# Performance work log

Measured on AMD Instinct MI355X. Metric: run time of the kernel, lower is better.

## Reference

```python
import jax, jax.numpy as jnp
import numpy as np

B, N, F, T, K, O = 8, 1024, 64, 32, 3, 64


def setup_inputs() -> dict:
    key = jax.random.key(0)
    k0, k1, k2, k3 = jax.random.split(key, 4)
    x = jax.random.normal(k0, (B, N, F, T), dtype=jnp.float32)
    spatial_attention = jax.random.uniform(k1, (B, N, N), dtype=jnp.float32)
    cheb = jax.random.normal(k2, (K, N, N), dtype=jnp.float32) * 0.1  # stacked T_k
    Theta = jax.random.normal(k3, (K, F, O), dtype=jnp.float32) * (1.0 / np.sqrt(F))
    return {"x": x, "spatial_attention": spatial_attention, "cheb": cheb, "Theta": Theta}


def reference(x, spatial_attention, cheb, Theta):
    # Original per-timestep, per-k loop computes:
    #   rhs[b,i,f] = sum_j (T_k[j,i] * att[b,j,i])... note: T_k_with_at.permute(0,2,1) @ x
    #   i.e. rhs[b,i,f,t] = sum_j T_k[j,i]*att[b,j,i]*x[b,j,f,t]
    # Vectorized over all timesteps t and Chebyshev orders k at once.
    rhs = jnp.einsum('kji,bji,bjft->bkift', cheb, spatial_attention, x)  # (B,K,N,F,T)
    out = jnp.einsum('bkift,kfo->biot', rhs, Theta)                      # sum over k,f
    return jax.nn.relu(out)  # (B,N,O,T)
```

## Files before the change

### kernel.cpp

```cpp
#include <hip/hip_runtime.h>
#include <stdint.h>

#define Bn 8
#define Nn 1024
#define Fn 64
#define Tn 32
#define Kn 3
#define On 64
#define Rn (Kn * Nn)
#define Cn (On * Tn)
#define NT (Rn / 64)

typedef __bf16 bf16x8 __attribute__((ext_vector_type(8)));
typedef float f32x4 __attribute__((ext_vector_type(4)));
typedef __attribute__((address_space(1))) void gvoid;
typedef __attribute__((address_space(3))) void lvoid;

union BF8 { bf16x8 v; ushort s[8]; uint4 q; };

static __device__ __forceinline__ ushort f2bf(float f) {
  uint32_t u = __float_as_uint(f);
  return (ushort)((u + 0x7FFFu + ((u >> 16) & 1u)) >> 16);
}

static __device__ __forceinline__ void glds(const ushort* g, ushort* l) {
  __builtin_amdgcn_global_load_lds((gvoid*)g, (lvoid*)l, 16, 0, 0);
}

__global__ void k_thetaT(const float* __restrict__ Theta, ushort* __restrict__ ThT) {
  int idx = blockIdx.x * 256 + threadIdx.x;
  if (idx < Kn * On * Fn) {
    int k = idx / (On * Fn);
    int rem = idx % (On * Fn);
    int o = rem / Fn, f = rem % Fn;
    ThT[idx] = f2bf(Theta[(k * Fn + f) * On + o]);
  }
}

__global__ __launch_bounds__(256) void k_prepW(const float* __restrict__ att,
                                               const float* __restrict__ cheb,
                                               ushort* __restrict__ Wt) {
  __shared__ float chebT[Kn][64][33];
  __shared__ float attT[64][33];
  int i0 = blockIdx.x * 64, j0 = blockIdx.y * 32;
  int tid = threadIdx.x;
  int il = tid & 63, jr = tid >> 6;
  int jc = tid & 3, iw = tid >> 2;

#pragma unroll
  for (int k = 0; k < Kn; k++)
#pragma unroll
    for (int p = 0; p < 8; p++) {
      int j = jr + p * 4;
      chebT[k][il][j] = cheb[((size_t)k * Nn + j0 + j) * Nn + i0 + il];
    }

  for (int b = 0; b < Bn; b++) {
    __syncthreads();
#pragma unroll
    for (int p = 0; p < 8; p++) {
      int j = jr + p * 4;
      attT[il][j] = att[((size_t)b * Nn + j0 + j) * Nn + i0 + il];
    }
    __syncthreads();
#pragma unroll
    for (int k = 0; k < Kn; k++) {
      ushort tmp[8];
#pragma unroll
      for (int q = 0; q < 8; q++)
        tmp[q] = f2bf(attT[iw][jc * 8 + q] * chebT[k][iw][jc * 8 + q]);
      *(uint4*)&Wt[((size_t)b * Nn + i0 + iw) * Rn + (size_t)k * Nn + j0 + jc * 8] =
          *(const uint4*)tmp;
    }
  }
}

__global__ __launch_bounds__(512) void k_prepY(const float* __restrict__ x,
                                               const ushort* __restrict__ ThT,
                                               ushort* __restrict__ Yt) {
  __shared__ ushort ylds[1024 * 32];
  int jt = blockIdx.x, b = blockIdx.y;
  int j0 = jt * 32;
  int tid = threadIdx.x;
  int lane = tid & 63, w = tid >> 6;
  int l15 = lane & 15, l4 = lane >> 4;

  BF8 bfr[4][2][2];
#pragma unroll
  for (int jj = 0; jj < 4; jj++) {
    const float* xp = x + ((size_t)b * Nn + (j0 + w * 4 + jj)) * (Fn * Tn);
#pragma unroll
    for (int ks = 0; ks < 2; ks++)
#pragma unroll
      for (int tf = 0; tf < 2; tf++) {
        int t = tf * 16 + l15;
        int fb = ks * 32 + l4 * 8;
#pragma unroll
        for (int e = 0; e < 8; e++)
          bfr[jj][ks][tf].s[e] = f2bf(xp[(fb + e) * Tn + t]);
      }
  }

  for (int k = 0; k < Kn; k++) {
    for (int h = 0; h < 2; h++) {
      BF8 afr[2][2];
#pragma unroll
      for (int o2 = 0; o2 < 2; o2++)
#pragma unroll
        for (int ks = 0; ks < 2; ks++) {
          int o = h * 32 + o2 * 16 + l15;
          afr[o2][ks].q = *(const uint4*)&ThT[((size_t)k * On + o) * Fn + ks * 32 + l4 * 8];
        }
#pragma unroll
      for (int jj = 0; jj < 4; jj++) {
        f32x4 acc[2][2] = {};
#pragma unroll
        for (int ks = 0; ks < 2; ks++)
#pragma unroll
          for (int o2 = 0; o2 < 2; o2++)
#pragma unroll
            for (int tf = 0; tf < 2; tf++)
              acc[o2][tf] = __builtin_amdgcn_mfma_f32_16x16x32_bf16(
                  afr[o2][ks].v, bfr[jj][ks][tf].v, acc[o2][tf], 0, 0, 0);
#pragma unroll
        for (int o2 = 0; o2 < 2; o2++)
#pragma unroll
          for (int tf = 0; tf < 2; tf++)
#pragma unroll
            for (int q = 0; q < 4; q++) {
              int cl = (o2 * 16 + l4 * 4 + q) * Tn + tf * 16 + l15;
              ylds[cl * 32 + w * 4 + jj] = f2bf(acc[o2][tf][q]);
            }
      }
      __syncthreads();
      const uint4* yl4 = (const uint4*)ylds;
      uint4* Yt4 = (uint4*)Yt;
      int e4 = tid & 3, r4 = tid >> 2;
      for (int pass = 0; pass < 8; pass++) {
        int cl = pass * 128 + r4;
        size_t off = ((size_t)b * Cn + (size_t)(h * 1024 + cl)) * Rn + (size_t)k * Nn + j0;
        Yt4[off / 8 + e4] = yl4[cl * 4 + e4];
      }
      __syncthreads();
    }
  }
}

__global__ __launch_bounds__(512, 2) void k_gemm(const ushort* __restrict__ Wt,
                                                 const ushort* __restrict__ Yt,
                                                 float* __restrict__ out) {
  extern __shared__ __align__(16) ushort smem[];
  ushort* As = smem;
  ushort* Bs = smem + 32768;

  int g = blockIdx.x;
  int b = g & 7, slot = g >> 3;
  int i0 = (slot & 3) * 256, c0 = (slot >> 2) * 256;
  int tid = threadIdx.x, lane = tid & 63, w = tid >> 6;
  int l15 = lane & 15, l4 = lane >> 4;
  int wm = w >> 2, wn = w & 3;

  const ushort* Ab = Wt + ((size_t)b * Nn + i0) * Rn;
  const ushort* Bb = Yt + ((size_t)b * Cn + c0) * Rn;

  int srcC = (((lane & 7) ^ (lane >> 3)) * 8);
  int arow0 = w * 8 + (lane >> 3);
  int brow0 = (w >> 2) * 64 + (w & 3) * 8 + (lane >> 3);

  int aL = (wm * 64 + l15) * 64;
  int bL = (wn * 32 + l15) * 64;
  int x7 = l15 & 7;
  int colx0 = ((l4) ^ x7) * 8;
  int colx1 = ((4 + l4) ^ x7) * 8;

  f32x4 acc[8][4] = {};
  BF8 afX[4][2], afY[4][2];
  BF8 bfX[2][2], bfY[2][2];

#define MFMA_(a_, b_, c_) __builtin_amdgcn_mfma_f32_16x16x32_bf16((a_), (b_), (c_), 0, 0, 0)
#define BAR() asm volatile("s_barrier" ::: "memory")
#define PRIO1 __builtin_amdgcn_s_setprio(1)
#define PRIO0 __builtin_amdgcn_s_setprio(0)
#define VMC(n_) asm volatile("s_waitcnt vmcnt(" #n_ ")" ::: "memory")

#define STAGE_A(t_, h_) { int bo_ = ((t_) & 1) * 16384 + (h_) * 8192 + w * 512; \
    const ushort* gp_ = Ab + (size_t)(arow0 + (h_) * 64) * Rn + (t_) * 64 + srcC; \
    glds(gp_, As + bo_); \
    glds(gp_ + 128 * (size_t)Rn, As + bo_ + 4096); }
#define STAGE_B(t_, h_) { int bo_ = ((t_) & 1) * 16384 + (h_) * 8192 + w * 512; \
    const ushort* gp_ = Bb + (size_t)(brow0 + (h_) * 32) * Rn + (t_) * 64 + srcC; \
    glds(gp_, Bs + bo_); \
    glds(gp_ + 128 * (size_t)Rn, Bs + bo_ + 4096); }

#define RD_A(DST_, bo_, mh_) { _Pragma("unroll") for (int m = 0; m < 4; m++) { \
    int ba_ = (bo_) + (mh_) * 8192 + aL + m * 1024; \
    DST_[m][0].q = *(const uint4*)&As[ba_ + colx0]; \
    DST_[m][1].q = *(const uint4*)&As[ba_ + colx1]; } }
#define RD_B(DST_, bo_, nh_) { _Pragma("unroll") for (int n = 0; n < 2; n++) { \
    int bb_ = (bo_) + (nh_) * 8192 + bL + n * 1024; \
    DST_[n][0].q = *(const uint4*)&Bs[bb_ + colx0]; \
    DST_[n][1].q = *(const uint4*)&Bs[bb_ + colx1]; } }

#define MMC(AF_, BF_, MO_, NO_) { _Pragma("unroll") for (int ks = 0; ks < 2; ks++) \
    _Pragma("unroll") for (int m = 0; m < 4; m++) \
      _Pragma("unroll") for (int n = 0; n < 2; n++) \
        acc[(MO_) + m][(NO_) + n] = MFMA_(AF_[m][ks].v, BF_[n][ks].v, acc[(MO_) + m][(NO_) + n]); }

  STAGE_A(0, 0); STAGE_B(0, 0); STAGE_B(0, 1); STAGE_A(0, 1); STAGE_A(1, 0);
  VMC(6); BAR();
  RD_A(afX, 0, 0); RD_B(bfX, 0, 0);

#define TILE(t_, S0_, S1_, S2_, W0_, W1_, W3_, LAST_) { \
    int bo_c = ((t_) & 1) * 16384; \
    VMC(W0_); BAR(); \
    RD_B(bfY, bo_c, 1); \
    if (S0_) STAGE_B((t_) + 1, 0); \
    PRIO1; MMC(afX, bfX, 0, 0); PRIO0; \
    VMC(W1_); BAR(); \
    RD_A(afY, bo_c, 1); \
    if (S1_) { STAGE_B((t_) + 1, 1); STAGE_A((t_) + 1, 1); } \
    PRIO1; MMC(afX, bfY, 0, 2); PRIO0; \
    if (S2_) STAGE_A((t_) + 2, 0); \
    PRIO1; MMC(afY, bfX, 4, 0); PRIO0; \
    if (!(LAST_)) { VMC(W3_); BAR(); \
      RD_A(afX, bo_c ^ 16384, 0); RD_B(bfX, bo_c ^ 16384, 0); } \
    PRIO1; MMC(afY, bfY, 4, 2); PRIO0; \
  }

  for (int t = 0; t < NT - 2; ++t)
    TILE(t, 1, 1, 1, 4, 4, 6, 0);
  TILE(NT - 2, 1, 1, 0, 4, 4, 4, 0);
  TILE(NT - 1, 0, 0, 0, 2, 0, 0, 1);

#undef TILE
#undef MMC
#undef RD_B
#undef RD_A
#undef STAGE_B
#undef STAGE_A
#undef VMC

  float* ob = out + (size_t)b * Nn * Cn;
#pragma unroll
  for (int m = 0; m < 8; m++) {
    int i = i0 + wm * 128 + m * 16 + l4 * 4;
#pragma unroll
    for (int n = 0; n < 4; n++) {
      int c = c0 + wn * 64 + n * 16 + l15;
#pragma unroll
      for (int q = 0; q < 4; q++)
        ob[(size_t)(i + q) * Cn + c] = fmaxf(acc[m][n][q], 0.0f);
    }
  }
}

extern "C" void kernel_launch(void* const* d_in, const int* in_sizes, int n_in,
                              void* d_out, int out_size, void* d_ws, size_t ws_size,
                              hipStream_t stream) {
  const float* x     = (const float*)d_in[0];
  const float* att   = (const float*)d_in[1];
  const float* cheb  = (const float*)d_in[2];
  const float* Theta = (const float*)d_in[3];
  float* out = (float*)d_out;

  char* ws = (char*)d_ws;
  ushort* ThT = (ushort*)ws;
  ushort* Wt  = (ushort*)(ws + 65536);
  ushort* Yt  = (ushort*)(ws + 65536 + 50331648ull);

  hipFuncSetAttribute((const void*)k_gemm, hipFuncAttributeMaxDynamicSharedMemorySize, 131072);

  k_thetaT<<<48, 256, 0, stream>>>(Theta, ThT);
  k_prepW<<<dim3(16, 32), 256, 0, stream>>>(att, cheb, Wt);
  k_prepY<<<dim3(32, 8), 512, 0, stream>>>(x, ThT, Yt);
  k_gemm<<<256, 512, 131072, stream>>>(Wt, Yt, out);
}
```

Baseline: 156.3 us.

## Merge W and Y prep kernels into one interleaved launch

Combines the separate k_prepW and k_prepY kernels into a single k_prep launch of 512 blocks. Odd blocks build the bf16 attention-weighted Chebyshev matrix and even blocks compute the Theta-projected x, so both independent streams run concurrently instead of back to back. The W tile grows from 64x32 to 64x64 with 512 threads, halving its block count, and dynamic shared memory is sized for the larger of the two roles. This removes one launch and the serialisation gap between kernels, but gives every block 65 KB of LDS, which can lower occupancy for the W role.

```diff
diff --git a/kernel.cpp b/kernel.cpp
--- a/kernel.cpp
+++ b/kernel.cpp
@@ -37,51 +37,57 @@
   }
 }
 
-__global__ __launch_bounds__(256) void k_prepW(const float* __restrict__ att,
-                                               const float* __restrict__ cheb,
-                                               ushort* __restrict__ Wt) {
-  __shared__ float chebT[Kn][64][33];
-  __shared__ float attT[64][33];
-  int i0 = blockIdx.x * 64, j0 = blockIdx.y * 32;
+__global__ __launch_bounds__(512) void k_prep(const float* __restrict__ att,
+                                              const float* __restrict__ cheb,
+                                              const float* __restrict__ x,
+                                              const ushort* __restrict__ ThT,
+                                              ushort* __restrict__ Wt,
+                                              ushort* __restrict__ Yt) {
+  extern __shared__ __align__(16) char psmem[];
+  int bid = blockIdx.x;
   int tid = threadIdx.x;
-  int il = tid & 63, jr = tid >> 6;
-  int jc = tid & 3, iw = tid >> 2;
-
-#pragma unroll
-  for (int k = 0; k < Kn; k++)
-#pragma unroll
-    for (int p = 0; p < 8; p++) {
-      int j = jr + p * 4;
-      chebT[k][il][j] = cheb[((size_t)k * Nn + j0 + j) * Nn + i0 + il];
+
+  if (bid & 1) {
+    int wb = bid >> 1;
+    float* chebT = (float*)psmem;
+    float* attT  = chebT + 3 * 64 * 65;
+    int i0 = (wb & 15) * 64, j0 = (wb >> 4) * 64;
+    int il = tid & 63, jr = tid >> 6;
+    int jc = tid & 7, iw = tid >> 3;
+
+#pragma unroll
+    for (int k = 0; k < Kn; k++)
+#pragma unroll
+      for (int p = 0; p < 8; p++) {
+        int j = jr + p * 8;
+        chebT[(k * 64 + il) * 65 + j] = cheb[((size_t)k * Nn + j0 + j) * Nn + i0 + il];
+      }
+
+    for (int b = 0; b < Bn; b++) {
+      __syncthreads();
+#pragma unroll
+      for (int p = 0; p < 8; p++) {
+        int j = jr + p * 8;
+        attT[il * 65 + j] = att[((size_t)b * Nn + j0 + j) * Nn + i0 + il];
+      }
+      __syncthreads();
+#pragma unroll
+      for (int k = 0; k < Kn; k++) {
+        ushort tmp[8];
+#pragma unroll
+        for (int q = 0; q < 8; q++)
+          tmp[q] = f2bf(attT[iw * 65 + jc * 8 + q] * chebT[(k * 64 + iw) * 65 + jc * 8 + q]);
+        *(uint4*)&Wt[((size_t)b * Nn + i0 + iw) * Rn + (size_t)k * Nn + j0 + jc * 8] =
+            *(const uint4*)tmp;
+      }
     }
-
-  for (int b = 0; b < Bn; b++) {
-    __syncthreads();
-#pragma unroll
-    for (int p = 0; p < 8; p++) {
-      int j = jr + p * 4;
-      attT[il][j] = att[((size_t)b * Nn + j0 + j) * Nn + i0 + il];
-    }
-    __syncthreads();
-#pragma unroll
-    for (int k = 0; k < Kn; k++) {
-      ushort tmp[8];
-#pragma unroll
-      for (int q = 0; q < 8; q++)
-        tmp[q] = f2bf(attT[iw][jc * 8 + q] * chebT[k][iw][jc * 8 + q]);
-      *(uint4*)&Wt[((size_t)b * Nn + i0 + iw) * Rn + (size_t)k * Nn + j0 + jc * 8] =
-          *(const uint4*)tmp;
-    }
-  }
-}
-
-__global__ __launch_bounds__(512) void k_prepY(const float* __restrict__ x,
-                                               const ushort* __restrict__ ThT,
-                                               ushort* __restrict__ Yt) {
-  __shared__ ushort ylds[1024 * 32];
-  int jt = blockIdx.x, b = blockIdx.y;
+    return;
+  }
+
+  ushort* ylds = (ushort*)psmem;
+  int yb = bid >> 1;
+  int jt = yb & 31, b = yb >> 5;
   int j0 = jt * 32;
-  int tid = threadIdx.x;
   int lane = tid & 63, w = tid >> 6;
   int l15 = lane & 15, l4 = lane >> 4;
 
@@ -268,10 +274,10 @@
   ushort* Wt  = (ushort*)(ws + 65536);
   ushort* Yt  = (ushort*)(ws + 65536 + 50331648ull);
 
+  hipFuncSetAttribute((const void*)k_prep, hipFuncAttributeMaxDynamicSharedMemorySize, 66560);
   hipFuncSetAttribute((const void*)k_gemm, hipFuncAttributeMaxDynamicSharedMemorySize, 131072);
 
   k_thetaT<<<48, 256, 0, stream>>>(Theta, ThT);
-  k_prepW<<<dim3(16, 32), 256, 0, stream>>>(att, cheb, Wt);
-  k_prepY<<<dim3(32, 8), 512, 0, stream>>>(x, ThT, Yt);
+  k_prep<<<512, 512, 66560, stream>>>(att, cheb, x, ThT, Wt, Yt);
   k_gemm<<<256, 512, 131072, stream>>>(Wt, Yt, out);
 }
```

Measured after the change: 158.2 us. No clear change (+1.2%).

## Restructure GEMM main loop into four-phase ping-pong schedule and pack LDS stores

Applied to the files above, without the earlier changes.

The main GEMM loop changes from a two-fragment-set schedule to a four-phase schedule. Each phase reads two A fragments and reuses all four B fragments, and each phase is bracketed by barriers and an LDS wait so global-to-LDS prefetches are spread across phases. This cuts fragment registers and aims to interleave memory and MFMA work more regularly. The Y-producing kernel now computes two j-columns together and writes packed 32-bit bf16 pairs to LDS, halving the number of LDS store instructions. The extra barriers per tile may add sync overhead, and the changed prefetch wait counts and stage ordering may be fragile.

```diff
diff --git a/kernel.cpp b/kernel.cpp
--- a/kernel.cpp
+++ b/kernel.cpp
@@ -111,17 +111,20 @@
           int o = h * 32 + o2 * 16 + l15;
           afr[o2][ks].q = *(const uint4*)&ThT[((size_t)k * On + o) * Fn + ks * 32 + l4 * 8];
         }
-#pragma unroll
-      for (int jj = 0; jj < 4; jj++) {
-        f32x4 acc[2][2] = {};
-#pragma unroll
-        for (int ks = 0; ks < 2; ks++)
-#pragma unroll
-          for (int o2 = 0; o2 < 2; o2++)
-#pragma unroll
-            for (int tf = 0; tf < 2; tf++)
-              acc[o2][tf] = __builtin_amdgcn_mfma_f32_16x16x32_bf16(
-                  afr[o2][ks].v, bfr[jj][ks][tf].v, acc[o2][tf], 0, 0, 0);
+      uint32_t* y32 = (uint32_t*)ylds;
+#pragma unroll
+      for (int jp = 0; jp < 2; jp++) {
+        f32x4 acc[2][2][2] = {};
+#pragma unroll
+        for (int j2 = 0; j2 < 2; j2++)
+#pragma unroll
+          for (int ks = 0; ks < 2; ks++)
+#pragma unroll
+            for (int o2 = 0; o2 < 2; o2++)
+#pragma unroll
+              for (int tf = 0; tf < 2; tf++)
+                acc[j2][o2][tf] = __builtin_amdgcn_mfma_f32_16x16x32_bf16(
+                    afr[o2][ks].v, bfr[jp * 2 + j2][ks][tf].v, acc[j2][o2][tf], 0, 0, 0);
 #pragma unroll
         for (int o2 = 0; o2 < 2; o2++)
 #pragma unroll
@@ -129,7 +132,9 @@
 #pragma unroll
             for (int q = 0; q < 4; q++) {
               int cl = (o2 * 16 + l4 * 4 + q) * Tn + tf * 16 + l15;
-              ylds[cl * 32 + w * 4 + jj] = f2bf(acc[o2][tf][q]);
+              uint32_t pk = (uint32_t)f2bf(acc[0][o2][tf][q]) |
+                            ((uint32_t)f2bf(acc[1][o2][tf][q]) << 16);
+              y32[cl * 16 + w * 2 + jp] = pk;
             }
       }
       __syncthreads();
@@ -174,11 +179,12 @@
   int colx1 = ((4 + l4) ^ x7) * 8;
 
   f32x4 acc[8][4] = {};
-  BF8 afX[4][2], afY[4][2];
-  BF8 bfX[2][2], bfY[2][2];
+  BF8 af[2][2];
+  BF8 bf[4][2];
 
 #define MFMA_(a_, b_, c_) __builtin_amdgcn_mfma_f32_16x16x32_bf16((a_), (b_), (c_), 0, 0, 0)
 #define BAR() asm volatile("s_barrier" ::: "memory")
+#define LGK0() asm volatile("s_waitcnt lgkmcnt(0)" ::: "memory")
 #define PRIO1 __builtin_amdgcn_s_setprio(1)
 #define PRIO0 __builtin_amdgcn_s_setprio(0)
 #define VMC(n_) asm volatile("s_waitcnt vmcnt(" #n_ ")" ::: "memory")
@@ -192,53 +198,55 @@
     glds(gp_, Bs + bo_); \
     glds(gp_ + 128 * (size_t)Rn, Bs + bo_ + 4096); }
 
-#define RD_A(DST_, bo_, mh_) { _Pragma("unroll") for (int m = 0; m < 4; m++) { \
-    int ba_ = (bo_) + (mh_) * 8192 + aL + m * 1024; \
-    DST_[m][0].q = *(const uint4*)&As[ba_ + colx0]; \
-    DST_[m][1].q = *(const uint4*)&As[ba_ + colx1]; } }
-#define RD_B(DST_, bo_, nh_) { _Pragma("unroll") for (int n = 0; n < 2; n++) { \
-    int bb_ = (bo_) + (nh_) * 8192 + bL + n * 1024; \
-    DST_[n][0].q = *(const uint4*)&Bs[bb_ + colx0]; \
-    DST_[n][1].q = *(const uint4*)&Bs[bb_ + colx1]; } }
-
-#define MMC(AF_, BF_, MO_, NO_) { _Pragma("unroll") for (int ks = 0; ks < 2; ks++) \
-    _Pragma("unroll") for (int m = 0; m < 4; m++) \
-      _Pragma("unroll") for (int n = 0; n < 2; n++) \
-        acc[(MO_) + m][(NO_) + n] = MFMA_(AF_[m][ks].v, BF_[n][ks].v, acc[(MO_) + m][(NO_) + n]); }
-
-  STAGE_A(0, 0); STAGE_B(0, 0); STAGE_B(0, 1); STAGE_A(0, 1); STAGE_A(1, 0);
+#define RD_A2(mp_, bo_) { _Pragma("unroll") for (int mm = 0; mm < 2; mm++) { \
+    int ba_ = (bo_) + ((mp_) >> 1) * 8192 + aL + (((mp_) & 1) * 2 + mm) * 1024; \
+    af[mm][0].q = *(const uint4*)&As[ba_ + colx0]; \
+    af[mm][1].q = *(const uint4*)&As[ba_ + colx1]; } }
+#define RD_B_ALL(bo_) { _Pragma("unroll") for (int n = 0; n < 4; n++) { \
+    int bb_ = (bo_) + (n >> 1) * 8192 + bL + (n & 1) * 1024; \
+    bf[n][0].q = *(const uint4*)&Bs[bb_ + colx0]; \
+    bf[n][1].q = *(const uint4*)&Bs[bb_ + colx1]; } }
+#define MM2(mp_) { _Pragma("unroll") for (int ks = 0; ks < 2; ks++) \
+    _Pragma("unroll") for (int mm = 0; mm < 2; mm++) \
+      _Pragma("unroll") for (int n = 0; n < 4; n++) \
+        acc[(mp_) * 2 + mm][n] = MFMA_(af[mm][ks].v, bf[n][ks].v, acc[(mp_) * 2 + mm][n]); }
+
+  STAGE_A(0, 0); STAGE_B(0, 0); STAGE_B(0, 1); STAGE_A(0, 1);
+  STAGE_A(1, 0); STAGE_B(1, 0); STAGE_B(1, 1);
   VMC(6); BAR();
-  RD_A(afX, 0, 0); RD_B(bfX, 0, 0);
-
-#define TILE(t_, S0_, S1_, S2_, W0_, W1_, W3_, LAST_) { \
-    int bo_c = ((t_) & 1) * 16384; \
-    VMC(W0_); BAR(); \
-    RD_B(bfY, bo_c, 1); \
-    if (S0_) STAGE_B((t_) + 1, 0); \
-    PRIO1; MMC(afX, bfX, 0, 0); PRIO0; \
-    VMC(W1_); BAR(); \
-    RD_A(afY, bo_c, 1); \
-    if (S1_) { STAGE_B((t_) + 1, 1); STAGE_A((t_) + 1, 1); } \
-    PRIO1; MMC(afX, bfY, 0, 2); PRIO0; \
-    if (S2_) STAGE_A((t_) + 2, 0); \
-    PRIO1; MMC(afY, bfX, 4, 0); PRIO0; \
-    if (!(LAST_)) { VMC(W3_); BAR(); \
-      RD_A(afX, bo_c ^ 16384, 0); RD_B(bfX, bo_c ^ 16384, 0); } \
-    PRIO1; MMC(afY, bfY, 4, 2); PRIO0; \
-  }
-
-  for (int t = 0; t < NT - 2; ++t)
-    TILE(t, 1, 1, 1, 4, 4, 6, 0);
-  TILE(NT - 2, 1, 1, 0, 4, 4, 4, 0);
-  TILE(NT - 1, 0, 0, 0, 2, 0, 0, 1);
+
+#define TILE(t_, SA1_, SN2_, WTAIL_) { \
+    int cur = ((t_) & 1) * 16384; \
+     \
+    RD_A2(0, cur); RD_B_ALL(cur); \
+    if (SA1_) STAGE_A((t_) + 1, 1); \
+    BAR(); LGK0(); PRIO1; MM2(0); PRIO0; BAR(); \
+     \
+    RD_A2(1, cur); \
+    if (SN2_) STAGE_A((t_) + 2, 0); \
+    BAR(); LGK0(); PRIO1; MM2(1); PRIO0; BAR(); \
+     \
+    RD_A2(2, cur); \
+    if (SN2_) STAGE_B((t_) + 2, 0); \
+    BAR(); LGK0(); PRIO1; MM2(2); PRIO0; BAR(); \
+     \
+    RD_A2(3, cur); \
+    if (SN2_) STAGE_B((t_) + 2, 1); \
+    WTAIL_; \
+    BAR(); LGK0(); PRIO1; MM2(3); PRIO0; BAR(); \
+  }
+
+  for (int t = 0; t <= NT - 3; ++t)
+    TILE(t, 1, 1, VMC(6));
+  TILE(NT - 2, 1, 0, VMC(0));
+  TILE(NT - 1, 0, 0, (void)0);
 
 #undef TILE
-#undef MMC
-#undef RD_B
-#undef RD_A
+#undef MM2
+#undef RD_B_ALL
+#undef RD_A2
 #undef STAGE_B
 #undef STAGE_A
-#undef VMC
 
   float* ob = out + (size_t)b * Nn * Cn;
 #pragma unroll
```

After: 181.0 us. +15.8%, slower.
